# Kernel optimization log

Hardware: AMD Instinct MI355X
Metric: run time of the kernel (lower is better)

Reference implementation:

```python
import jax, jax.numpy as jnp
import numpy as np

EPS = 1e-12  # F.normalize eps
NUM_CLASSES = 80


def _l2_normalize(x, axis):
    # matches torch F.normalize: x / max(||x||_2, eps)
    n = jnp.sqrt(jnp.sum(x * x, axis=axis, keepdims=True))
    return x / jnp.maximum(n, EPS)


def setup_inputs() -> dict:
    key = jax.random.key(0)
    k1, k2, k3, k4 = jax.random.split(key, 4)
    B, C, H, W = 16, 256, 128, 128
    N = NUM_CLASSES
    features = jax.random.normal(k1, (B, C, H, W), dtype=jnp.float32)
    centroids = jax.random.normal(k2, (N, C), dtype=jnp.float32)
    fc_w = jax.random.normal(k3, (C, C, 1, 1), dtype=jnp.float32) * 0.02
    fc_b = jax.random.normal(k4, (C,), dtype=jnp.float32) * 0.01
    return {"features": features, "centroids": centroids, "fc_w": fc_w, "fc_b": fc_b}


def reference(features, centroids, fc_w, fc_b):
    N = centroids.shape[0]
    # cosine similarity to class centroids: [B, N, H, W]
    sim = jnp.einsum('bchw,nc->bnhw', _l2_normalize(features, axis=1),
                     _l2_normalize(centroids, axis=1))
    # hard one-hot assignment along class dim (scatter of argmax)
    idx = jnp.argmax(sim, axis=1)                              # [B, H, W]
    mask = jax.nn.one_hot(idx, N, axis=1, dtype=features.dtype)  # [B, N, H, W]
    # per-image, per-class mean feature (gather/blend)
    sum_x = jnp.einsum('bnhw,bchw->bnc', mask, features)       # [B, N, C]
    count = jnp.sum(mask, axis=(2, 3))[:, :, None]             # [B, N, 1]
    cent = sum_x / jnp.maximum(count, 1.0)
    delta = jnp.einsum('bnhw,bnc->bchw', mask, cent) - features
    alpha = jnp.exp(-jnp.mean(jnp.square(delta), axis=1, keepdims=True))  # [B,1,H,W]
    x = features + alpha * delta
    # 1x1 conv == channel matmul
    out = jnp.einsum('bchw,oc->bohw', x, fc_w[:, :, 0, 0]) + fc_b[None, :, None, None]
    return jax.nn.relu(out)
```

## Files before the change

### kernel.cpp

```cpp
#include <hip/hip_runtime.h>


typedef __bf16 bf16x8 __attribute__((ext_vector_type(8)));
typedef float  f32x4  __attribute__((ext_vector_type(4)));
typedef unsigned char u8;

__device__ __forceinline__ unsigned short f2b(float f) {
  unsigned u = __float_as_uint(f);
  return (unsigned short)((u + 0x7fffu + ((u >> 16) & 1u)) >> 16);
}
__device__ __forceinline__ float b2f(unsigned short s) {
  return __uint_as_float((unsigned)s << 16);
}

__global__ __launch_bounds__(256) void k0_cnorm(const float* __restrict__ cent,
                                                float* __restrict__ cnT,
                                                int* __restrict__ cntg) {
  int n = blockIdx.x, t = threadIdx.x;
  if (t < 16) cntg[n * 16 + t] = 0;
  float v = cent[n * 256 + t];
  float s = v * v;
  #pragma unroll
  for (int o = 32; o > 0; o >>= 1) s += __shfl_down(s, o, 64);
  __shared__ float red[4];
  if ((t & 63) == 0) red[t >> 6] = s;
  __syncthreads();
  float tot = red[0] + red[1] + red[2] + red[3];
  float dn = fmaxf(sqrtf(tot), 1e-12f);
  cnT[t * 80 + n] = v / dn;
}

__global__ __launch_bounds__(256) void k0_wprep(const float* __restrict__ fcw,
                                                unsigned short* __restrict__ wks,
                                                float* __restrict__ wt,
                                                int* __restrict__ sumxi) {
  int o = blockIdx.x, c = threadIdx.x;
  float w = fcw[o * 256 + c];
  wt[c * 256 + o] = w;
  wks[((c >> 5) * 256 + o) * 32 + (c & 31)] = f2b(w);
  for (int i = o * 256 + c; i < 16 * 80 * 256; i += 65536) sumxi[i] = 0;
}

__global__ __launch_bounds__(256) void k1f(const float* __restrict__ feat,
                                           const float* __restrict__ cnT,
                                           u8* __restrict__ idxb,
                                           float* __restrict__ fsqg,
                                           int* __restrict__ cntg,
                                           int* __restrict__ sumxi) {
  __shared__ alignas(8) u8 idxl[256];
  __shared__ int lh[80];
  const int bid = blockIdx.x;
  const int b = bid >> 5, kp = bid & 31;
  const int t = threadIdx.x, wv = t >> 6, ln = t & 63, lo = ln & 15, hi = ln >> 4;

  f32x4 acc[5][4];
  f32x4 zz = {0.f, 0.f, 0.f, 0.f};
  #pragma unroll
  for (int mt = 0; mt < 5; ++mt)
    #pragma unroll
    for (int nt = 0; nt < 4; ++nt) acc[mt][nt] = zz;
  if (t < 80) lh[t] = 0;

  for (int cc = 0; cc < 2; ++cc) {
    const int px0 = kp * 512 + cc * 256;
    __syncthreads();

    const float* fb = feat + (size_t)b * 256 * 16384 + px0 + t;
    float g[80];
    #pragma unroll
    for (int n = 0; n < 80; ++n) g[n] = 0.f;
    float fsq = 0.f;
    #pragma unroll 4
    for (int c = 0; c < 256; ++c) {
      float v = fb[(size_t)c * 16384];
      fsq = fmaf(v, v, fsq);
      const float* cr = cnT + c * 80;
      #pragma unroll
      for (int n = 0; n < 80; ++n) g[n] = fmaf(v, cr[n], g[n]);
    }
    float best = g[0]; int bi = 0;
    #pragma unroll
    for (int n = 1; n < 80; ++n) if (g[n] > best) { best = g[n]; bi = n; }
    idxb[b * 16384 + px0 + t] = (u8)bi;
    fsqg[b * 16384 + px0 + t] = fsq;
    idxl[t] = (u8)bi;
    atomicAdd(&lh[bi], 1);
    __syncthreads();

    const int chb = wv * 64;
    #pragma unroll 2
    for (int ks = 0; ks < 8; ++ks) {
      uint2 iv = *(const uint2*)&idxl[ks * 32 + hi * 8];
      int id[8];
      #pragma unroll
      for (int j = 0; j < 4; ++j) { id[j] = (iv.x >> (8 * j)) & 255; id[4 + j] = (iv.y >> (8 * j)) & 255; }
      bf16x8 bfr[4];
      #pragma unroll
      for (int nt = 0; nt < 4; ++nt) {
        const float* bp = feat + ((size_t)b * 256 + chb + nt * 16 + lo) * 16384 + px0 + ks * 32 + hi * 8;
        float4 v0 = *(const float4*)bp;
        float4 v1 = *(const float4*)(bp + 4);
        union { unsigned short u[8]; bf16x8 v; } bb;
        bb.u[0] = f2b(v0.x); bb.u[1] = f2b(v0.y); bb.u[2] = f2b(v0.z); bb.u[3] = f2b(v0.w);
        bb.u[4] = f2b(v1.x); bb.u[5] = f2b(v1.y); bb.u[6] = f2b(v1.z); bb.u[7] = f2b(v1.w);
        bfr[nt] = bb.v;
      }
      #pragma unroll
      for (int mt = 0; mt < 5; ++mt) {
        int row = mt * 16 + lo;
        union { unsigned short u[8]; bf16x8 v; } ma;
        #pragma unroll
        for (int j = 0; j < 8; ++j) ma.u[j] = (id[j] == row) ? (unsigned short)0x3F80 : (unsigned short)0;
        #pragma unroll
        for (int nt = 0; nt < 4; ++nt)
          acc[mt][nt] = __builtin_amdgcn_mfma_f32_16x16x32_bf16(ma.v, bfr[nt], acc[mt][nt], 0, 0, 0);
      }
    }
  }
  __syncthreads();
  if (t < 80) atomicAdd(&cntg[b * 80 + t], lh[t]);
  #pragma unroll
  for (int mt = 0; mt < 5; ++mt)
    #pragma unroll
    for (int nt = 0; nt < 4; ++nt)
      #pragma unroll
      for (int r = 0; r < 4; ++r) {
        int cls = mt * 16 + hi * 4 + r;
        int ch = wv * 64 + nt * 16 + lo;
        atomicAdd(&sumxi[((size_t)b * 80 + cls) * 256 + ch],
                  __float2int_rn(acc[mt][nt][r] * 8192.f));
      }
}

__global__ __launch_bounds__(256) void k2_cent(const int* __restrict__ sumxi,
                                               const int* __restrict__ cntg,
                                               const float* __restrict__ wt,
                                               unsigned short* __restrict__ centf,
                                               float* __restrict__ csqg,
                                               float* __restrict__ chatg) {
  int bn = blockIdx.x; int t = threadIdx.x;
  float dn = fmaxf((float)cntg[bn], 1.0f);
  float cv = (float)sumxi[(size_t)bn * 256 + t] * (1.0f / 8192.0f) / dn;
  __shared__ float cl[256];
  __shared__ float red[4];
  cl[t] = cv;
  centf[(size_t)bn * 256 + t] = f2b(cv);
  float q = cv * cv;
  #pragma unroll
  for (int o = 32; o > 0; o >>= 1) q += __shfl_down(q, o, 64);
  if ((t & 63) == 0) red[t >> 6] = q;
  __syncthreads();
  if (t == 0) csqg[bn] = red[0] + red[1] + red[2] + red[3];
  float acc = 0.f;
  #pragma unroll 4
  for (int c = 0; c < 256; ++c) acc = fmaf(wt[c * 256 + t], cl[c], acc);
  chatg[(size_t)bn * 256 + t] = acc;
}

__global__ __launch_bounds__(512) void k3b_gemm(const float* __restrict__ feat,
    const u8* __restrict__ idxb, const float* __restrict__ fsqg,
    const float* __restrict__ csqg, const unsigned short* __restrict__ centf,
    const float* __restrict__ chatg, const unsigned short* __restrict__ wks,
    const float* __restrict__ fcb, float* __restrict__ out) {
  __shared__ alignas(16) unsigned short featT[2][64 * 264];
  __shared__ float alphal[64];
  const int t = threadIdx.x;
  const int w = t >> 6, ln = t & 63, lo = ln & 15, hi = ln >> 4;
  const int pl = ln, cph = w;

  bf16x8 wf[2][8];
  #pragma unroll
  for (int ml = 0; ml < 2; ++ml)
    #pragma unroll
    for (int ks = 0; ks < 8; ++ks)
      wf[ml][ks] = *(const bf16x8*)&wks[((size_t)ks * 256 + (w * 2 + ml) * 16 + lo) * 32 + hi * 8];
  f32x4 bias2[2];
  #pragma unroll
  for (int ml = 0; ml < 2; ++ml)
    bias2[ml] = *(const f32x4*)&fcb[w * 32 + ml * 16 + hi * 4];

  const int tile0 = blockIdx.x * 8;
  {
    int b = tile0 >> 8, p0 = (tile0 & 255) << 6;
    const float* fb = feat + ((size_t)b * 256 + cph * 32) * 16384 + p0 + pl;
    #pragma unroll
    for (int jj = 0; jj < 4; ++jj) {
      union { unsigned short u[8]; uint4 q; } pk;
      #pragma unroll
      for (int e = 0; e < 8; ++e) pk.u[e] = f2b(fb[(size_t)(jj * 8 + e) * 16384]);
      *(uint4*)&featT[0][pl * 264 + cph * 32 + jj * 8] = pk.q;
    }
  }

  float nxv[32];
  for (int rep = 0; rep < 8; ++rep) {
    const int cur = rep & 1;
    const int tile = tile0 + rep;
    const int b = tile >> 8, p0 = (tile & 255) << 6;

    __syncthreads();

    if (rep < 7) {
      int t2 = tile + 1;
      int b2 = t2 >> 8, p02 = (t2 & 255) << 6;
      const float* fb2 = feat + ((size_t)b2 * 256 + cph * 32) * 16384 + p02 + pl;
      #pragma unroll
      for (int e = 0; e < 32; ++e) nxv[e] = fb2[(size_t)e * 16384];
    }

    {
      int p = t >> 3, sub = t & 7;
      int cid = idxb[b * 16384 + p0 + p];
      const unsigned short* cw = centf + ((size_t)b * 80 + cid) * 256 + sub * 32;
      const unsigned short* fr = &featT[cur][p * 264 + sub * 32];
      float sel = 0.f;
      #pragma unroll
      for (int j = 0; j < 4; ++j) {
        uint4 cc = *(const uint4*)&cw[j * 8];
        uint4 ff = *(const uint4*)&fr[j * 8];
        sel = fmaf(b2f((unsigned short)(ff.x & 0xffff)), b2f((unsigned short)(cc.x & 0xffff)), sel);
        sel = fmaf(b2f((unsigned short)(ff.x >> 16)),    b2f((unsigned short)(cc.x >> 16)),    sel);
        sel = fmaf(b2f((unsigned short)(ff.y & 0xffff)), b2f((unsigned short)(cc.y & 0xffff)), sel);
        sel = fmaf(b2f((unsigned short)(ff.y >> 16)),    b2f((unsigned short)(cc.y >> 16)),    sel);
        sel = fmaf(b2f((unsigned short)(ff.z & 0xffff)), b2f((unsigned short)(cc.z & 0xffff)), sel);
        sel = fmaf(b2f((unsigned short)(ff.z >> 16)),    b2f((unsigned short)(cc.z >> 16)),    sel);
        sel = fmaf(b2f((unsigned short)(ff.w & 0xffff)), b2f((unsigned short)(cc.w & 0xffff)), sel);
        sel = fmaf(b2f((unsigned short)(ff.w >> 16)),    b2f((unsigned short)(cc.w >> 16)),    sel);
      }
      sel += __shfl_xor(sel, 1, 64);
      sel += __shfl_xor(sel, 2, 64);
      sel += __shfl_xor(sel, 4, 64);
      if (sub == 0) {
        float fsq = fsqg[b * 16384 + p0 + p];
        float msq = (csqg[b * 80 + cid] - 2.f * sel + fsq) * (1.f / 256.f);
        alphal[p] = expf(-msq);
      }
    }

    f32x4 acc[2][4];
    f32x4 zz = {0.f, 0.f, 0.f, 0.f};
    #pragma unroll
    for (int ml = 0; ml < 2; ++ml)
      #pragma unroll
      for (int pt = 0; pt < 4; ++pt) acc[ml][pt] = zz;

    #pragma unroll
    for (int ks = 0; ks < 8; ++ks) {
      bf16x8 bfr[4];
      #pragma unroll
      for (int pt = 0; pt < 4; ++pt)
        bfr[pt] = *(const bf16x8*)&featT[cur][(pt * 16 + lo) * 264 + ks * 32 + hi * 8];
      #pragma unroll
      for (int ml = 0; ml < 2; ++ml)
        #pragma unroll
        for (int pt = 0; pt < 4; ++pt)
          acc[ml][pt] = __builtin_amdgcn_mfma_f32_16x16x32_bf16(wf[ml][ks], bfr[pt], acc[ml][pt], 0, 0, 0);
    }
    __syncthreads();

    #pragma unroll
    for (int pt = 0; pt < 4; ++pt) {
      int plx = pt * 16 + lo;
      int p = p0 + plx;
      float a = alphal[plx];
      float om = 1.f - a;
      int cid = idxb[b * 16384 + p];
      const float* crow = chatg + ((size_t)b * 80 + cid) * 256;
      #pragma unroll
      for (int ml = 0; ml < 2; ++ml) {
        int o0 = w * 32 + ml * 16 + hi * 4;
        float4 c4 = *(const float4*)&crow[o0];
        size_t ob = ((size_t)b * 256 + o0) * 16384 + p;
        out[ob            ] = fmaxf(fmaf(a, c4.x, om * acc[ml][pt][0]) + bias2[ml][0], 0.f);
        out[ob + 16384    ] = fmaxf(fmaf(a, c4.y, om * acc[ml][pt][1]) + bias2[ml][1], 0.f);
        out[ob + 2 * 16384] = fmaxf(fmaf(a, c4.z, om * acc[ml][pt][2]) + bias2[ml][2], 0.f);
        out[ob + 3 * 16384] = fmaxf(fmaf(a, c4.w, om * acc[ml][pt][3]) + bias2[ml][3], 0.f);
      }
    }

    if (rep < 7) {
      #pragma unroll
      for (int jj = 0; jj < 4; ++jj) {
        union { unsigned short u[8]; uint4 q; } pk;
        #pragma unroll
        for (int e = 0; e < 8; ++e) pk.u[e] = f2b(nxv[jj * 8 + e]);
        *(uint4*)&featT[cur ^ 1][pl * 264 + cph * 32 + jj * 8] = pk.q;
      }
    }
  }
}

extern "C" void kernel_launch(void* const* d_in, const int* in_sizes, int n_in,
                              void* d_out, int out_size, void* d_ws, size_t ws_size,
                              hipStream_t stream) {
  (void)in_sizes; (void)n_in; (void)out_size; (void)ws_size;
  const float* feat = (const float*)d_in[0];
  const float* cent = (const float*)d_in[1];
  const float* fcw  = (const float*)d_in[2];
  const float* fcb  = (const float*)d_in[3];
  float* out = (float*)d_out;
  char* ws = (char*)d_ws;
  float* cnT             = (float*)(ws);
  float* wt              = (float*)(ws + 81920);
  unsigned short* wks    = (unsigned short*)(ws + 344064);
  unsigned short* centf  = (unsigned short*)(ws + 475136);
  u8*    idxb            = (u8*)(ws + 1130496);
  float* fsq             = (float*)(ws + 1392640);
  int*   cntg            = (int*)(ws + 2441216);
  float* csq             = (float*)(ws + 2446336);
  float* chat            = (float*)(ws + 2451456);
  int*   sumxi           = (int*)(ws + 3762176);

  k0_cnorm<<<80, 256, 0, stream>>>(cent, cnT, cntg);
  k0_wprep<<<256, 256, 0, stream>>>(fcw, wks, wt, sumxi);
  k1f<<<512, 256, 0, stream>>>(feat, cnT, idxb, fsq, cntg, sumxi);
  k2_cent<<<1280, 256, 0, stream>>>(sumxi, cntg, wt, centf, csq, chat);
  k3b_gemm<<<512, 512, 0, stream>>>(feat, idxb, fsq, csq, centf, chat, wks, fcb, out);
}
```

Measured before the change: 485.5 us.

## Replace atomic int class-sum accumulation with per-chunk float partials reduced in k2

```diff
diff --git a/kernel.cpp b/kernel.cpp
--- a/kernel.cpp
+++ b/kernel.cpp
@@ -32,13 +32,11 @@
 
 __global__ __launch_bounds__(256) void k0_wprep(const float* __restrict__ fcw,
                                                 unsigned short* __restrict__ wks,
-                                                float* __restrict__ wt,
-                                                int* __restrict__ sumxi) {
+                                                float* __restrict__ wt) {
   int o = blockIdx.x, c = threadIdx.x;
   float w = fcw[o * 256 + c];
   wt[c * 256 + o] = w;
   wks[((c >> 5) * 256 + o) * 32 + (c & 31)] = f2b(w);
-  for (int i = o * 256 + c; i < 16 * 80 * 256; i += 65536) sumxi[i] = 0;
 }
 
 __global__ __launch_bounds__(256) void k1f(const float* __restrict__ feat,
@@ -46,12 +44,38 @@
                                            u8* __restrict__ idxb,
                                            float* __restrict__ fsqg,
                                            int* __restrict__ cntg,
-                                           int* __restrict__ sumxi) {
+                                           float* __restrict__ part) {
   __shared__ alignas(8) u8 idxl[256];
   __shared__ int lh[80];
-  const int bid = blockIdx.x;
-  const int b = bid >> 5, kp = bid & 31;
+  const int b = blockIdx.x >> 6, chunk = blockIdx.x & 63;
+  const int px0 = chunk << 8;
   const int t = threadIdx.x, wv = t >> 6, ln = t & 63, lo = ln & 15, hi = ln >> 4;
+  if (t < 80) lh[t] = 0;
+  __syncthreads();
+
+  const int pi = px0 | t;
+  const float* fb = feat + (size_t)b * 256 * 16384 + pi;
+  float g[80];
+  #pragma unroll
+  for (int n = 0; n < 80; ++n) g[n] = 0.f;
+  float fsq = 0.f;
+  #pragma unroll 4
+  for (int c = 0; c < 256; ++c) {
+    float v = fb[(size_t)c * 16384];
+    fsq = fmaf(v, v, fsq);
+    const float* cr = cnT + c * 80;
+    #pragma unroll
+    for (int n = 0; n < 80; ++n) g[n] = fmaf(v, cr[n], g[n]);
+  }
+  float best = g[0]; int bi = 0;
+  #pragma unroll
+  for (int n = 1; n < 80; ++n) if (g[n] > best) { best = g[n]; bi = n; }
+  idxb[b * 16384 + pi] = (u8)bi;
+  fsqg[b * 16384 + pi] = fsq;
+  idxl[t] = (u8)bi;
+  atomicAdd(&lh[bi], 1);
+  __syncthreads();
+  if (t < 80) atomicAdd(&cntg[b * 80 + t], lh[t]);
 
   f32x4 acc[5][4];
   f32x4 zz = {0.f, 0.f, 0.f, 0.f};
@@ -59,88 +83,58 @@
   for (int mt = 0; mt < 5; ++mt)
     #pragma unroll
     for (int nt = 0; nt < 4; ++nt) acc[mt][nt] = zz;
-  if (t < 80) lh[t] = 0;
-
-  for (int cc = 0; cc < 2; ++cc) {
-    const int px0 = kp * 512 + cc * 256;
-    __syncthreads();
-
-    const float* fb = feat + (size_t)b * 256 * 16384 + px0 + t;
-    float g[80];
-    #pragma unroll
-    for (int n = 0; n < 80; ++n) g[n] = 0.f;
-    float fsq = 0.f;
-    #pragma unroll 4
-    for (int c = 0; c < 256; ++c) {
-      float v = fb[(size_t)c * 16384];
-      fsq = fmaf(v, v, fsq);
-      const float* cr = cnT + c * 80;
-      #pragma unroll
-      for (int n = 0; n < 80; ++n) g[n] = fmaf(v, cr[n], g[n]);
-    }
-    float best = g[0]; int bi = 0;
-    #pragma unroll
-    for (int n = 1; n < 80; ++n) if (g[n] > best) { best = g[n]; bi = n; }
-    idxb[b * 16384 + px0 + t] = (u8)bi;
-    fsqg[b * 16384 + px0 + t] = fsq;
-    idxl[t] = (u8)bi;
-    atomicAdd(&lh[bi], 1);
-    __syncthreads();
-
-    const int chb = wv * 64;
-    #pragma unroll 2
-    for (int ks = 0; ks < 8; ++ks) {
-      uint2 iv = *(const uint2*)&idxl[ks * 32 + hi * 8];
-      int id[8];
-      #pragma unroll
-      for (int j = 0; j < 4; ++j) { id[j] = (iv.x >> (8 * j)) & 255; id[4 + j] = (iv.y >> (8 * j)) & 255; }
-      bf16x8 bfr[4];
-      #pragma unroll
-      for (int nt = 0; nt < 4; ++nt) {
-        const float* bp = feat + ((size_t)b * 256 + chb + nt * 16 + lo) * 16384 + px0 + ks * 32 + hi * 8;
-        float4 v0 = *(const float4*)bp;
-        float4 v1 = *(const float4*)(bp + 4);
-        union { unsigned short u[8]; bf16x8 v; } bb;
-        bb.u[0] = f2b(v0.x); bb.u[1] = f2b(v0.y); bb.u[2] = f2b(v0.z); bb.u[3] = f2b(v0.w);
-        bb.u[4] = f2b(v1.x); bb.u[5] = f2b(v1.y); bb.u[6] = f2b(v1.z); bb.u[7] = f2b(v1.w);
-        bfr[nt] = bb.v;
-      }
-      #pragma unroll
-      for (int mt = 0; mt < 5; ++mt) {
-        int row = mt * 16 + lo;
-        union { unsigned short u[8]; bf16x8 v; } ma;
-        #pragma unroll
-        for (int j = 0; j < 8; ++j) ma.u[j] = (id[j] == row) ? (unsigned short)0x3F80 : (unsigned short)0;
-        #pragma unroll
-        for (int nt = 0; nt < 4; ++nt)
-          acc[mt][nt] = __builtin_amdgcn_mfma_f32_16x16x32_bf16(ma.v, bfr[nt], acc[mt][nt], 0, 0, 0);
-      }
+  const int chb = wv * 64;
+  #pragma unroll 2
+  for (int ks = 0; ks < 8; ++ks) {
+    uint2 iv = *(const uint2*)&idxl[ks * 32 + hi * 8];
+    int id[8];
+    #pragma unroll
+    for (int j = 0; j < 4; ++j) { id[j] = (iv.x >> (8 * j)) & 255; id[4 + j] = (iv.y >> (8 * j)) & 255; }
+    bf16x8 bfr[4];
+    #pragma unroll
+    for (int nt = 0; nt < 4; ++nt) {
+      const float* bp = feat + ((size_t)b * 256 + chb + nt * 16 + lo) * 16384 + px0 + ks * 32 + hi * 8;
+      float4 v0 = *(const float4*)bp;
+      float4 v1 = *(const float4*)(bp + 4);
+      union { unsigned short u[8]; bf16x8 v; } bb;
+      bb.u[0] = f2b(v0.x); bb.u[1] = f2b(v0.y); bb.u[2] = f2b(v0.z); bb.u[3] = f2b(v0.w);
+      bb.u[4] = f2b(v1.x); bb.u[5] = f2b(v1.y); bb.u[6] = f2b(v1.z); bb.u[7] = f2b(v1.w);
+      bfr[nt] = bb.v;
+    }
+    #pragma unroll
+    for (int mt = 0; mt < 5; ++mt) {
+      int row = mt * 16 + lo;
+      union { unsigned short u[8]; bf16x8 v; } ma;
+      #pragma unroll
+      for (int j = 0; j < 8; ++j) ma.u[j] = (id[j] == row) ? (unsigned short)0x3F80 : (unsigned short)0;
+      #pragma unroll
+      for (int nt = 0; nt < 4; ++nt)
+        acc[mt][nt] = __builtin_amdgcn_mfma_f32_16x16x32_bf16(ma.v, bfr[nt], acc[mt][nt], 0, 0, 0);
     }
   }
-  __syncthreads();
-  if (t < 80) atomicAdd(&cntg[b * 80 + t], lh[t]);
+  float* pb = part + ((size_t)(b * 64 + chunk) * 80) * 256;
   #pragma unroll
   for (int mt = 0; mt < 5; ++mt)
     #pragma unroll
     for (int nt = 0; nt < 4; ++nt)
       #pragma unroll
-      for (int r = 0; r < 4; ++r) {
-        int cls = mt * 16 + hi * 4 + r;
-        int ch = wv * 64 + nt * 16 + lo;
-        atomicAdd(&sumxi[((size_t)b * 80 + cls) * 256 + ch],
-                  __float2int_rn(acc[mt][nt][r] * 8192.f));
-      }
-}
-
-__global__ __launch_bounds__(256) void k2_cent(const int* __restrict__ sumxi,
+      for (int r = 0; r < 4; ++r)
+        pb[(mt * 16 + hi * 4 + r) * 256 + chb + nt * 16 + lo] = acc[mt][nt][r];
+}
+
+__global__ __launch_bounds__(256) void k2_cent(const float* __restrict__ part,
                                                const int* __restrict__ cntg,
                                                const float* __restrict__ wt,
                                                unsigned short* __restrict__ centf,
                                                float* __restrict__ csqg,
                                                float* __restrict__ chatg) {
-  int bn = blockIdx.x; int t = threadIdx.x;
+  int bn = blockIdx.x; int b = bn / 80, n = bn - b * 80; int t = threadIdx.x;
   float dn = fmaxf((float)cntg[bn], 1.0f);
-  float cv = (float)sumxi[(size_t)bn * 256 + t] * (1.0f / 8192.0f) / dn;
+  float s = 0.f;
+  const float* pp = part + ((size_t)(b * 64) * 80 + n) * 256 + t;
+  #pragma unroll 8
+  for (int ck = 0; ck < 64; ++ck) s += pp[(size_t)ck * 80 * 256];
+  float cv = s / dn;
   __shared__ float cl[256];
   __shared__ float red[4];
   cl[t] = cv;
@@ -164,6 +158,7 @@
     const float* __restrict__ fcb, float* __restrict__ out) {
   __shared__ alignas(16) unsigned short featT[2][64 * 264];
   __shared__ float alphal[64];
+  __shared__ int cidl[64];
   const int t = threadIdx.x;
   const int w = t >> 6, ln = t & 63, lo = ln & 15, hi = ln >> 4;
   const int pl = ln, cph = w;
@@ -234,6 +229,7 @@
         float fsq = fsqg[b * 16384 + p0 + p];
         float msq = (csqg[b * 80 + cid] - 2.f * sel + fsq) * (1.f / 256.f);
         alphal[p] = expf(-msq);
+        cidl[p] = cid;
       }
     }
 
@@ -264,8 +260,7 @@
       int p = p0 + plx;
       float a = alphal[plx];
       float om = 1.f - a;
-      int cid = idxb[b * 16384 + p];
-      const float* crow = chatg + ((size_t)b * 80 + cid) * 256;
+      const float* crow = chatg + ((size_t)b * 80 + cidl[plx]) * 256;
       #pragma unroll
       for (int ml = 0; ml < 2; ++ml) {
         int o0 = w * 32 + ml * 16 + hi * 4;
@@ -309,11 +304,11 @@
   int*   cntg            = (int*)(ws + 2441216);
   float* csq             = (float*)(ws + 2446336);
   float* chat            = (float*)(ws + 2451456);
-  int*   sumxi           = (int*)(ws + 3762176);
+  float* part            = (float*)(ws + 3762176);
 
   k0_cnorm<<<80, 256, 0, stream>>>(cent, cnT, cntg);
-  k0_wprep<<<256, 256, 0, stream>>>(fcw, wks, wt, sumxi);
-  k1f<<<512, 256, 0, stream>>>(feat, cnT, idxb, fsq, cntg, sumxi);
-  k2_cent<<<1280, 256, 0, stream>>>(sumxi, cntg, wt, centf, csq, chat);
+  k0_wprep<<<256, 256, 0, stream>>>(fcw, wks, wt);
+  k1f<<<1024, 256, 0, stream>>>(feat, cnT, idxb, fsq, cntg, part);
+  k2_cent<<<1280, 256, 0, stream>>>(part, cntg, wt, centf, csq, chat);
   k3b_gemm<<<512, 512, 0, stream>>>(feat, idxb, fsq, csq, centf, chat, wks, fcb, out);
 }
```

New measurement: 490.5 us. Within noise of the previous version (+1.0%).
